# Performance work log

Hardware: AMD Instinct MI355X
Metric: run time of the kernel (lower is better)

## Reference

```python
import jax, jax.numpy as jnp
import numpy as np
from jax import lax

NBINS = 10
PP = 8            # pixels_per_cell
CPB = 2           # cells_per_block
MAX_ANGLE = float(np.pi)
EPS = 1e-5


def setup_inputs() -> dict:
    key = jax.random.key(0)
    img = jax.random.uniform(key, (32, 1, 512, 512), dtype=jnp.float32)
    # fixed Sobel-like gradient filters, same as the torch buffer: (2,1,3,3) OIHW
    m = np.array([[1.0, 0.0, -1.0], [2.0, 0.0, -2.0], [1.0, 0.0, -1.0]], dtype=np.float32)
    weight = jnp.asarray(np.stack([m, m.T])[:, None, :, :])
    return {"img": img, "weight": weight}


def reference(img, weight):
    n, _, H, W = img.shape
    # gradient conv: padding=1, stride=1 keeps spatial size
    gxy = lax.conv_general_dilated(
        img, weight, window_strides=(1, 1), padding=[(1, 1), (1, 1)],
        dimension_numbers=("NCHW", "OIHW", "NCHW"))  # (n,2,H,W)
    mag = jnp.sqrt(jnp.sum(gxy * gxy, axis=1))          # (n,H,W)
    phase = jnp.arctan2(gxy[:, 0], gxy[:, 1])           # (n,H,W)
    pbin = phase / MAX_ANGLE * NBINS
    fl = jnp.floor(pbin).astype(jnp.int32) % NBINS
    ce = jnp.ceil(pbin).astype(jnp.int32) % NBINS
    # scatter_ sets mag at floor bin (out starts at zeros), scatter_add_ adds (1-mag) at ceil bin
    oh_fl = jax.nn.one_hot(fl, NBINS, dtype=img.dtype)  # (n,H,W,nbins)
    oh_ce = jax.nn.one_hot(ce, NBINS, dtype=img.dtype)
    out = oh_fl * mag[..., None] + oh_ce * (1.0 - mag)[..., None]
    out = jnp.moveaxis(out, -1, 1)                      # (n,nbins,H,W)
    # avg pool with kernel==stride==PP, no padding -> reshape mean
    hc, wc = H // PP, W // PP
    out = out.reshape(n, NBINS, hc, PP, wc, PP).mean(axis=(3, 5))  # (n,nbins,hc,wc)
    # block normalization (L2-Hys); note: norms reduce over batch dim too, as in the source
    nbr, nbc = hc - CPB + 1, wc - CPB + 1
    blocks = jnp.stack(
        [jnp.stack([out[:, :, i:i + nbr, j:j + nbc] for j in range(CPB)], axis=2)
         for i in range(CPB)], axis=2)                  # (n,nbins,CPB,CPB,nbr,nbc)
    s = jnp.sum(blocks * blocks, axis=(0, 1, 2, 3), keepdims=True)
    v = blocks / jnp.sqrt(s + EPS * EPS)
    v = jnp.minimum(v, 0.2)
    s2 = jnp.sum(v * v, axis=(0, 1, 2, 3), keepdims=True)
    v = v / jnp.sqrt(s2 + EPS * EPS)
    return v.reshape(n, -1)  # feature_vector=True
```

## Files before the change

### kernel.cpp

```cpp
#include <hip/hip_runtime.h>
#include <math.h>

#define NBINS 10
#define NB    32
#define HH    512
#define WW    512
#define HC    64
#define WC    64
#define NBR   63
#define NBC   63
#define EPS2  1e-10

__global__ __launch_bounds__(256) void k_cellhist(const float* __restrict__ img,
                                                  float* __restrict__ cell) {
    const int cy = blockIdx.x;
    const int n  = blockIdx.y;
    const int t  = threadIdx.x;

    __shared__ float lds[10][516];

    const float* im = img + (size_t)n * HH * WW;
    const int gy0 = cy * 8 - 1;
    for (int idx = t; idx < 10 * 514; idx += 256) {
        int r  = idx / 514;
        int c  = idx - r * 514;
        int gr = gy0 + r, gc = c - 1;
        float v = 0.0f;
        if ((unsigned)gr < HH && (unsigned)gc < WW) v = im[gr * WW + gc];
        lds[r][c] = v;
    }
    __syncthreads();

    float hist[NBINS];
#pragma unroll
    for (int b = 0; b < NBINS; ++b) hist[b] = 0.0f;

    const float pi32 = (float)M_PI;
    const int cc   = t >> 2;
    const int sub  = t & 3;
    const int r0   = 1 + 2 * sub;
    const int stag = 2 * ((t >> 4) & 3) + sub;

    for (int ry = 0; ry < 2; ++ry) {
        const int row = r0 + ry;
        for (int k = 0; k < 8; ++k) {
            const int px  = (k + stag) & 7;
            const int col = cc * 8 + px + 1;
            float a  = lds[row - 1][col - 1];
            float b  = lds[row - 1][col    ];
            float c  = lds[row - 1][col + 1];
            float d  = lds[row    ][col - 1];
            float f  = lds[row    ][col + 1];
            float g  = lds[row + 1][col - 1];
            float h  = lds[row + 1][col    ];
            float i2 = lds[row + 1][col + 1];
            float gA = a;
            gA = gA - c;
            gA = gA + 2.0f * d;
            gA = gA - 2.0f * f;
            gA = gA + g;
            gA = gA - i2;
            float gB = a;
            gB = gB + 2.0f * b;
            gB = gB + c;
            gB = gB - g;
            gB = gB - 2.0f * h;
            gB = gB - i2;

            float mag = sqrtf(gA * gA + gB * gB);

            float pbf = atan2f(gA, gB);
            pbf = pbf / pi32;
            pbf = pbf * 10.0f;
            float fr  = floorf(pbf);
            float dfr = pbf - fr;
            int fl, ce;
            if (dfr > 1e-4f && dfr < 0.9999f) {
                fl = (int)fr;
                ce = fl + 1;
            } else {
                float phase = (float)atan2((double)gA, (double)gB);
                float pb = phase / pi32;
                pb = pb * 10.0f;
                fl = (int)floorf(pb);
                ce = (int)ceilf(pb);
            }
            int flm = fl % NBINS; if (flm < 0) flm += NBINS;
            int cem = ce % NBINS; if (cem < 0) cem += NBINS;
            hist[flm] += mag;
            hist[cem] += 1.0f - mag;
        }
    }

#pragma unroll
    for (int b = 0; b < NBINS; ++b) {
        hist[b] += __shfl_xor(hist[b], 1);
        hist[b] += __shfl_xor(hist[b], 2);
    }

#pragma unroll
    for (int bb = 0; bb < NBINS; ++bb) {
        if ((bb & 3) == sub)
            cell[(((size_t)n * NBINS + bb) * HC + cy) * WC + cc] = hist[bb] * 0.015625f;
    }
}

__global__ __launch_bounds__(64) void k_Q(const float* __restrict__ cell,
                                          double* __restrict__ Q) {
    const int i     = blockIdx.x;
    const int chunk = blockIdx.y;
    const int j     = threadIdx.x;
    double acc = 0.0;
    for (int nb = chunk * 32; nb < chunk * 32 + 32; ++nb) {
        double v = (double)cell[((size_t)nb * HC + i) * WC + j];
        acc += v * v;
    }
    atomicAdd(&Q[i * WC + j], acc);
}

__global__ __launch_bounds__(64) void k_s2(const float* __restrict__ cell,
                                           const double* __restrict__ Q,
                                           double* __restrict__ s2) {
    const int i     = blockIdx.x;
    const int chunk = blockIdx.y;
    const int j     = threadIdx.x;
    if (j >= NBC) return;
    double s = Q[i * WC + j] + Q[i * WC + j + 1] +
               Q[(i + 1) * WC + j] + Q[(i + 1) * WC + j + 1];
    double w = 1.0 / sqrt(s + EPS2);
    double acc = 0.0;
    for (int nb = chunk * 16; nb < chunk * 16 + 16; ++nb) {
#pragma unroll
        for (int di = 0; di < 2; ++di)
#pragma unroll
            for (int dj = 0; dj < 2; ++dj) {
                double v = (double)cell[((size_t)nb * HC + i + di) * WC + j + dj] * w;
                v = fmin(v, 0.2);
                acc += v * v;
            }
    }
    atomicAdd(&s2[i * NBC + j], acc);
}

__global__ void k_out(const float* __restrict__ cell,
                      const double* __restrict__ Q,
                      const double* __restrict__ s2,
                      float* __restrict__ out) {
    int idx = blockIdx.x * blockDim.x + threadIdx.x;
    const int total = NB * NBINS * 2 * 2 * NBR * NBC;
    if (idx >= total) return;
    int j   = idx % NBC;
    int tmp = idx / NBC;
    int i   = tmp % NBR; tmp /= NBR;
    int dj  = tmp % 2;   tmp /= 2;
    int di  = tmp % 2;   tmp /= 2;
    int b   = tmp % NBINS;
    int n   = tmp / NBINS;
    double s = Q[i * WC + j] + Q[i * WC + j + 1] +
               Q[(i + 1) * WC + j] + Q[(i + 1) * WC + j + 1];
    double inv1 = 1.0 / sqrt(s + EPS2);
    double inv2 = 1.0 / sqrt(s2[i * NBC + j] + EPS2);
    double v = (double)cell[(((size_t)n * NBINS + b) * HC + i + di) * WC + j + dj] * inv1;
    v = fmin(v, 0.2);
    out[idx] = (float)(v * inv2);
}

extern "C" void kernel_launch(void* const* d_in, const int* in_sizes, int n_in,
                              void* d_out, int out_size, void* d_ws, size_t ws_size,
                              hipStream_t stream) {
    const float* img = (const float*)d_in[0];
    float* out = (float*)d_out;

    float*  cell = (float*)d_ws;
    double* Q    = (double*)(cell + (size_t)NB * NBINS * HC * WC);
    double* s2   = Q + HC * WC;

    hipMemsetAsync(Q, 0, (size_t)(HC * WC + NBR * NBC) * sizeof(double), stream);
    hipLaunchKernelGGL(k_cellhist, dim3(HC, NB), dim3(256), 0, stream, img, cell);
    hipLaunchKernelGGL(k_Q, dim3(HC, 10), dim3(64), 0, stream, cell, Q);
    hipLaunchKernelGGL(k_s2, dim3(NBR, 20), dim3(64), 0, stream, cell, Q, s2);
    const int total = NB * NBINS * 2 * 2 * NBR * NBC;
    hipLaunchKernelGGL(k_out, dim3((total + 255) / 256), dim3(256), 0, stream,
                       cell, Q, s2, out);
}
```

Before: 147.8 us.

## Replace atan2 binning with sector cross-products, fuse Q into histogram, use fp32 norms

The per-pixel atan2f is replaced by sign tests against four fixed sector boundary directions, which gives the floor and ceil bins directly. The double-precision atan2 fallback is kept for pixels near a boundary. The per-cell sum of squares (Q) is now accumulated with atomics inside the histogram kernel, so the separate k_Q pass is removed. The normalization kernels switch from double to float, and a small kernel precomputes the inverse norms so k_out no longer recomputes them per element. The fp32 accumulation and atomic ordering may shift results slightly compared with the double-precision path.

```diff
diff --git a/kernel.cpp b/kernel.cpp
--- a/kernel.cpp
+++ b/kernel.cpp
@@ -9,10 +9,11 @@
 #define WC    64
 #define NBR   63
 #define NBC   63
-#define EPS2  1e-10
+#define EPS2F 1e-10f
 
 __global__ __launch_bounds__(256) void k_cellhist(const float* __restrict__ img,
-                                                  float* __restrict__ cell) {
+                                                  float* __restrict__ cell,
+                                                  float* __restrict__ Q) {
     const int cy = blockIdx.x;
     const int n  = blockIdx.y;
     const int t  = threadIdx.x;
@@ -36,6 +37,11 @@
     for (int b = 0; b < NBINS; ++b) hist[b] = 0.0f;
 
     const float pi32 = (float)M_PI;
+    const float S1 = 0.30901699f, C1 = 0.95105652f;
+    const float S2 = 0.58778525f, C2 = 0.80901699f;
+    const float S3 = 0.80901699f, C3 = 0.58778525f;
+    const float S4 = 0.95105652f, C4 = 0.30901699f;
+
     const int cc   = t >> 2;
     const int sub  = t & 3;
     const int r0   = 1 + 2 * sub;
@@ -69,24 +75,29 @@
 
             float mag = sqrtf(gA * gA + gB * gB);
 
-            float pbf = atan2f(gA, gB);
-            pbf = pbf / pi32;
-            pbf = pbf * 10.0f;
-            float fr  = floorf(pbf);
-            float dfr = pbf - fr;
-            int fl, ce;
-            if (dfr > 1e-4f && dfr < 0.9999f) {
-                fl = (int)fr;
-                ce = fl + 1;
+            float y = fabsf(gA), x = fabsf(gB);
+            float cr1 = fmaf(y, C1, -(x * S1));
+            float cr2 = fmaf(y, C2, -(x * S2));
+            float cr3 = fmaf(y, C3, -(x * S3));
+            float cr4 = fmaf(y, C4, -(x * S4));
+            int idx = (cr1 > 0.0f) + (cr2 > 0.0f) + (cr3 > 0.0f) + (cr4 > 0.0f);
+            float minc = fminf(fminf(y, x),
+                               fminf(fminf(fabsf(cr1), fabsf(cr2)),
+                                     fminf(fabsf(cr3), fabsf(cr4))));
+            int flm, cem;
+            if (minc > 3.2e-5f * mag) {
+                bool same = (gA >= 0.0f) == (gB >= 0.0f);
+                flm = same ? idx : 9 - idx;
+                cem = same ? idx + 1 : (idx ? 10 - idx : 0);
             } else {
                 float phase = (float)atan2((double)gA, (double)gB);
                 float pb = phase / pi32;
                 pb = pb * 10.0f;
-                fl = (int)floorf(pb);
-                ce = (int)ceilf(pb);
+                int fl = (int)floorf(pb);
+                int ce = (int)ceilf(pb);
+                flm = fl % NBINS; if (flm < 0) flm += NBINS;
+                cem = ce % NBINS; if (cem < 0) cem += NBINS;
             }
-            int flm = fl % NBINS; if (flm < 0) flm += NBINS;
-            int cem = ce % NBINS; if (cem < 0) cem += NBINS;
             hist[flm] += mag;
             hist[cem] += 1.0f - mag;
         }
@@ -103,66 +114,72 @@
         if ((bb & 3) == sub)
             cell[(((size_t)n * NBINS + bb) * HC + cy) * WC + cc] = hist[bb] * 0.015625f;
     }
-}
-
-__global__ __launch_bounds__(64) void k_Q(const float* __restrict__ cell,
-                                          double* __restrict__ Q) {
+    if (sub == 0) {
+        float q = 0.0f;
+#pragma unroll
+        for (int bb = 0; bb < NBINS; ++bb) {
+            float cv = hist[bb] * 0.015625f;
+            q = fmaf(cv, cv, q);
+        }
+        atomicAdd(&Q[cy * WC + cc], q);
+    }
+}
+
+__global__ __launch_bounds__(256) void k_s2(const float* __restrict__ cell,
+                                            const float* __restrict__ Q,
+                                            float* __restrict__ s2) {
     const int i     = blockIdx.x;
     const int chunk = blockIdx.y;
-    const int j     = threadIdx.x;
-    double acc = 0.0;
-    for (int nb = chunk * 32; nb < chunk * 32 + 32; ++nb) {
-        double v = (double)cell[((size_t)nb * HC + i) * WC + j];
-        acc += v * v;
-    }
-    atomicAdd(&Q[i * WC + j], acc);
-}
-
-__global__ __launch_bounds__(64) void k_s2(const float* __restrict__ cell,
-                                           const double* __restrict__ Q,
-                                           double* __restrict__ s2) {
-    const int i     = blockIdx.x;
-    const int chunk = blockIdx.y;
-    const int j     = threadIdx.x;
+    const int t     = threadIdx.x;
+    const int j     = t & 63;
+    const int sub   = t >> 6;
     if (j >= NBC) return;
-    double s = Q[i * WC + j] + Q[i * WC + j + 1] +
-               Q[(i + 1) * WC + j] + Q[(i + 1) * WC + j + 1];
-    double w = 1.0 / sqrt(s + EPS2);
-    double acc = 0.0;
-    for (int nb = chunk * 16; nb < chunk * 16 + 16; ++nb) {
-#pragma unroll
-        for (int di = 0; di < 2; ++di)
-#pragma unroll
-            for (int dj = 0; dj < 2; ++dj) {
-                double v = (double)cell[((size_t)nb * HC + i + di) * WC + j + dj] * w;
-                v = fmin(v, 0.2);
-                acc += v * v;
-            }
+    float s = Q[i * WC + j] + Q[i * WC + j + 1] +
+              Q[(i + 1) * WC + j] + Q[(i + 1) * WC + j + 1];
+    float w = 1.0f / sqrtf(s + EPS2F);
+    float acc = 0.0f;
+    const int nb0 = (chunk * 4 + sub) * 10;
+    for (int nb = nb0; nb < nb0 + 10; ++nb) {
+        const float* base = cell + ((size_t)nb * HC + i) * WC + j;
+        float v00 = base[0], v01 = base[1];
+        float v10 = base[WC], v11 = base[WC + 1];
+        v00 = fminf(v00 * w, 0.2f); acc = fmaf(v00, v00, acc);
+        v01 = fminf(v01 * w, 0.2f); acc = fmaf(v01, v01, acc);
+        v10 = fminf(v10 * w, 0.2f); acc = fmaf(v10, v10, acc);
+        v11 = fminf(v11 * w, 0.2f); acc = fmaf(v11, v11, acc);
     }
     atomicAdd(&s2[i * NBC + j], acc);
 }
 
+__global__ void k_inv(const float* __restrict__ Q, const float* __restrict__ s2,
+                      float* __restrict__ inv1, float* __restrict__ inv2) {
+    int idx = blockIdx.x * blockDim.x + threadIdx.x;
+    if (idx >= NBR * NBC) return;
+    int i = idx / NBC, j = idx - i * NBC;
+    float s = Q[i * WC + j] + Q[i * WC + j + 1] +
+              Q[(i + 1) * WC + j] + Q[(i + 1) * WC + j + 1];
+    inv1[idx] = 1.0f / sqrtf(s + EPS2F);
+    inv2[idx] = 1.0f / sqrtf(s2[idx] + EPS2F);
+}
+
 __global__ void k_out(const float* __restrict__ cell,
-                      const double* __restrict__ Q,
-                      const double* __restrict__ s2,
+                      const float* __restrict__ inv1,
+                      const float* __restrict__ inv2,
                       float* __restrict__ out) {
     int idx = blockIdx.x * blockDim.x + threadIdx.x;
     const int total = NB * NBINS * 2 * 2 * NBR * NBC;
     if (idx >= total) return;
-    int j   = idx % NBC;
-    int tmp = idx / NBC;
-    int i   = tmp % NBR; tmp /= NBR;
+    int ij  = idx % (NBR * NBC);
+    int tmp = idx / (NBR * NBC);
+    int j   = ij % NBC;
+    int i   = ij / NBC;
     int dj  = tmp % 2;   tmp /= 2;
     int di  = tmp % 2;   tmp /= 2;
     int b   = tmp % NBINS;
     int n   = tmp / NBINS;
-    double s = Q[i * WC + j] + Q[i * WC + j + 1] +
-               Q[(i + 1) * WC + j] + Q[(i + 1) * WC + j + 1];
-    double inv1 = 1.0 / sqrt(s + EPS2);
-    double inv2 = 1.0 / sqrt(s2[i * NBC + j] + EPS2);
-    double v = (double)cell[(((size_t)n * NBINS + b) * HC + i + di) * WC + j + dj] * inv1;
-    v = fmin(v, 0.2);
-    out[idx] = (float)(v * inv2);
+    float v = cell[(((size_t)n * NBINS + b) * HC + i + di) * WC + j + dj] * inv1[ij];
+    v = fminf(v, 0.2f);
+    out[idx] = v * inv2[ij];
 }
 
 extern "C" void kernel_launch(void* const* d_in, const int* in_sizes, int n_in,
@@ -171,15 +188,17 @@
     const float* img = (const float*)d_in[0];
     float* out = (float*)d_out;
 
-    float*  cell = (float*)d_ws;
-    double* Q    = (double*)(cell + (size_t)NB * NBINS * HC * WC);
-    double* s2   = Q + HC * WC;
-
-    hipMemsetAsync(Q, 0, (size_t)(HC * WC + NBR * NBC) * sizeof(double), stream);
-    hipLaunchKernelGGL(k_cellhist, dim3(HC, NB), dim3(256), 0, stream, img, cell);
-    hipLaunchKernelGGL(k_Q, dim3(HC, 10), dim3(64), 0, stream, cell, Q);
-    hipLaunchKernelGGL(k_s2, dim3(NBR, 20), dim3(64), 0, stream, cell, Q, s2);
+    float* cell = (float*)d_ws;
+    float* Q    = cell + (size_t)NB * NBINS * HC * WC;
+    float* s2   = Q + HC * WC;
+    float* inv1 = s2 + NBR * NBC;
+    float* inv2 = inv1 + NBR * NBC;
+
+    hipMemsetAsync(Q, 0, (size_t)(HC * WC + NBR * NBC) * sizeof(float), stream);
+    hipLaunchKernelGGL(k_cellhist, dim3(HC, NB), dim3(256), 0, stream, img, cell, Q);
+    hipLaunchKernelGGL(k_s2, dim3(NBR, 8), dim3(256), 0, stream, cell, Q, s2);
+    hipLaunchKernelGGL(k_inv, dim3(16), dim3(256), 0, stream, Q, s2, inv1, inv2);
     const int total = NB * NBINS * 2 * 2 * NBR * NBC;
     hipLaunchKernelGGL(k_out, dim3((total + 255) / 256), dim3(256), 0, stream,
-                       cell, Q, s2, out);
-}
+                       cell, inv1, inv2, out);
+}
```

Result: faster. 132.8 us (-10.1%).
